# Performance work log

Hardware: AMD Instinct MI355X
Metric: run time of the kernel (lower is better)

The kernel has to match this reference:

```python
import jax, jax.numpy as jnp
import numpy as np

B, S, D, H = 8, 1024, 768, 12
DH = D // H


def setup_inputs() -> dict:
    key = jax.random.key(0)
    ks = jax.random.split(key, 6)
    scale = 1.0 / np.sqrt(D)
    return {
        "inputs": jax.random.normal(ks[0], (B, S, D), dtype=jnp.float32),
        "Wq": jax.random.normal(ks[1], (D, D), dtype=jnp.float32) * scale,
        "bq": jnp.zeros((D,), jnp.float32),
        "Wk": jax.random.normal(ks[2], (D, D), dtype=jnp.float32) * scale,
        "bk": jnp.zeros((D,), jnp.float32),
        "Wv": jax.random.normal(ks[3], (D, D), dtype=jnp.float32) * scale,
        "bv": jnp.zeros((D,), jnp.float32),
        "Wo": jax.random.normal(ks[4], (D, D), dtype=jnp.float32) * scale,
        "bo": jnp.zeros((D,), jnp.float32),
    }


def _split_heads(x):
    # [B,S,D] -> [B,H,S,DH]
    b, s, _ = x.shape
    return x.reshape(b, s, H, DH).transpose(0, 2, 1, 3)


def reference(inputs, Wq, bq, Wk, bk, Wv, bv, Wo, bo):
    q = _split_heads(inputs @ Wq + bq)
    k = _split_heads(inputs @ Wk + bk)
    v = _split_heads(inputs @ Wv + bv)
    # scaled dot-product attention; scale = sqrt(projection_dim)
    scores = jnp.einsum("bhqd,bhkd->bhqk", q, k) / jnp.sqrt(jnp.float32(DH))
    weights = jax.nn.softmax(scores, axis=-1)
    attn = jnp.einsum("bhqk,bhkd->bhqd", weights, v)
    attn = attn.transpose(0, 2, 1, 3).reshape(inputs.shape[0], -1, D)
    return attn @ Wo + bo
```

## Files before the change

### kernel.cpp

```cpp
#include <hip/hip_runtime.h>
#include <math.h>

#define B 8
#define S 1024
#define D 768
#define H 12
#define DH 64
#define M_TOT (B * S)

#define QSCALE 0.18033688011112042f

typedef short bf16x8 __attribute__((ext_vector_type(8)));
typedef float f32x4 __attribute__((ext_vector_type(4)));
typedef unsigned u32x4 __attribute__((ext_vector_type(4)));

__device__ __forceinline__ unsigned short f2bf(float x) {
    unsigned u = __builtin_bit_cast(unsigned, x);
    u = (u + 0x7FFFu + ((u >> 16) & 1u)) >> 16;
    return (unsigned short)u;
}
__device__ __forceinline__ unsigned short f2bf_ru(float x) {
    return (unsigned short)((__builtin_bit_cast(unsigned, x) + 0x8000u) >> 16);
}
__device__ __forceinline__ unsigned pk2bf_ru(float a, float b) {
    unsigned ua = __builtin_bit_cast(unsigned, a) + 0x8000u;
    unsigned ub = __builtin_bit_cast(unsigned, b) + 0x8000u;
    return __builtin_amdgcn_perm(ub, ua, 0x07060302u);
}

__device__ __forceinline__ void async16(const unsigned short* g, unsigned short* l) {
    __builtin_amdgcn_global_load_lds((const __attribute__((address_space(1))) void*)g,
                                     (__attribute__((address_space(3))) void*)l, 16, 0, 0);
}

__device__ __forceinline__ void stage_tiles(const unsigned short* __restrict__ A,
                                            const unsigned short* __restrict__ Bt,
                                            unsigned short* At, unsigned short* Bs,
                                            int m0, int n0, int k0, int w, int srow, int scol) {
#pragma unroll
    for (int c = 0; c < 2; ++c) {
        const int cc = w * 2 + c;
        const int row = cc * 16 + srow;
        async16(&A[(size_t)(m0 + row) * D + k0 + scol], &At[cc * 512]);
        async16(&Bt[(size_t)(n0 + row) * D + k0 + scol], &Bs[cc * 512]);
    }
}

__global__ __launch_bounds__(256) void prep(const float* __restrict__ inputs,
                                            unsigned short* __restrict__ Abf,
                                            const float* W0, const float* W1,
                                            const float* W2, const float* W3,
                                            unsigned short* T0, unsigned short* T1,
                                            unsigned short* T2, unsigned short* T3) {
    const int bid = blockIdx.x;
    const int t = threadIdx.x;
    if (bid < 6144) {
        const int i = (bid * 256 + t) * 4;
        const float4 v = *(const float4*)&inputs[i];
        ushort4 o;
        o.x = f2bf(v.x); o.y = f2bf(v.y); o.z = f2bf(v.z); o.w = f2bf(v.w);
        *(ushort4*)&Abf[i] = o;
    } else {
        const int id = bid - 6144;
        const int z = id / 144;
        const int rem = id % 144;
        const int kx = rem % 12, ny = rem / 12;
        const float* Wsrc[4] = {W0, W1, W2, W3};
        unsigned short* Tdst[4] = {T0, T1, T2, T3};
        const float* Wm = Wsrc[z];
        unsigned short* Tm = Tdst[z];
        __shared__ float tile[64][65];
        const int r = t >> 4, c4 = (t & 15) * 4;
        const int k0 = kx * 64, n0 = ny * 64;
#pragma unroll
        for (int rr = 0; rr < 4; ++rr) {
            const float4 v = *(const float4*)&Wm[(size_t)(k0 + r + rr * 16) * D + n0 + c4];
            tile[r + rr * 16][c4 + 0] = v.x;
            tile[r + rr * 16][c4 + 1] = v.y;
            tile[r + rr * 16][c4 + 2] = v.z;
            tile[r + rr * 16][c4 + 3] = v.w;
        }
        __syncthreads();
#pragma unroll
        for (int rr = 0; rr < 4; ++rr) {
            const int nr = r + rr * 16;
            ushort4 o;
            o.x = f2bf(tile[c4 + 0][nr]);
            o.y = f2bf(tile[c4 + 1][nr]);
            o.z = f2bf(tile[c4 + 2][nr]);
            o.w = f2bf(tile[c4 + 3][nr]);
            *(ushort4*)&Tm[(size_t)(n0 + nr) * D + k0 + c4] = o;
        }
    }
}

__global__ __launch_bounds__(256) void gemm_qkv(const unsigned short* __restrict__ A,
                                                const unsigned short* __restrict__ Wtq,
                                                const unsigned short* __restrict__ Wtk,
                                                const unsigned short* __restrict__ Wtv,
                                                const float* __restrict__ bq,
                                                const float* __restrict__ bk,
                                                const float* __restrict__ bv,
                                                unsigned short* __restrict__ Qb,
                                                unsigned short* __restrict__ Kb,
                                                unsigned short* __restrict__ Vtb) {
    __shared__ unsigned short At[2][128 * 32];
    __shared__ unsigned short Bs[2][128 * 32];
    const int z = blockIdx.z;
    const unsigned short* Bt = (z == 0) ? Wtq : (z == 1) ? Wtk : Wtv;
    const float* bias = (z == 0) ? bq : (z == 1) ? bk : bv;
    const float scale = (z == 0) ? QSCALE : 1.0f;

    const int t = threadIdx.x;
    const int w = t >> 6, lane = t & 63;
    const int quad = lane >> 4, l15 = lane & 15;
    const int m0 = blockIdx.x * 128, n0 = blockIdx.y * 128;
    const int wm = (w & 1) * 64, wn = (w >> 1) * 64;
    const int srow = lane >> 2, scol = (lane & 3) * 8;

    f32x4 acc[4][4];
#pragma unroll
    for (int i = 0; i < 4; ++i)
#pragma unroll
        for (int j = 0; j < 4; ++j) acc[i][j] = (f32x4){0.f, 0.f, 0.f, 0.f};

    stage_tiles(A, Bt, At[0], Bs[0], m0, n0, 0, w, srow, scol);
    for (int kt = 0; kt < D / 32; ++kt) {
        unsigned short* Atc = At[kt & 1];
        unsigned short* Bsc = Bs[kt & 1];
        if (kt + 1 < D / 32) {
            stage_tiles(A, Bt, At[(kt + 1) & 1], Bs[(kt + 1) & 1], m0, n0, (kt + 1) * 32, w, srow, scol);
            __asm__ volatile("s_waitcnt vmcnt(4)" ::: "memory");
        } else {
            __asm__ volatile("s_waitcnt vmcnt(0)" ::: "memory");
        }
        __asm__ volatile("s_barrier" ::: "memory");
        bf16x8 af[4], bfr[4];
#pragma unroll
        for (int i = 0; i < 4; ++i)
            af[i] = *(const bf16x8*)&Atc[(wm + i * 16 + l15) * 32 + quad * 8];
#pragma unroll
        for (int j = 0; j < 4; ++j)
            bfr[j] = *(const bf16x8*)&Bsc[(wn + j * 16 + l15) * 32 + quad * 8];
#pragma unroll
        for (int i = 0; i < 4; ++i)
#pragma unroll
            for (int j = 0; j < 4; ++j)
                acc[i][j] = __builtin_amdgcn_mfma_f32_16x16x32_bf16(af[i], bfr[j], acc[i][j], 0, 0, 0);
        __asm__ volatile("s_barrier" ::: "memory");
    }

#pragma unroll
    for (int j = 0; j < 4; ++j) {
        const int col = n0 + wn + j * 16 + l15;
        const float bv2 = bias[col];
#pragma unroll
        for (int i = 0; i < 4; ++i) {
            const int row0 = m0 + wm + i * 16 + quad * 4;
            if (z < 2) {
                unsigned short* C = (z == 0) ? Qb : Kb;
#pragma unroll
                for (int r = 0; r < 4; ++r)
                    C[(size_t)(row0 + r) * D + col] = f2bf_ru((acc[i][j][r] + bv2) * scale);
            } else {
                const int h = col >> 6, dh = col & 63;
                const int bb = row0 >> 10, s0 = row0 & 1023;
                const int g = (s0 & 63) >> 2;
                const int kap = ((g >> 3) << 5) | ((g & 3) << 3) | (((g >> 2) & 1) << 2);
                const int s0p = (s0 & ~63) | kap;
                uint2 u;
                u.x = pk2bf_ru(acc[i][j][0] + bv2, acc[i][j][1] + bv2);
                u.y = pk2bf_ru(acc[i][j][2] + bv2, acc[i][j][3] + bv2);
                *(uint2*)&Vtb[((size_t)(bb * H + h) * DH + dh) * S + s0p] = u;
            }
        }
    }
}

__global__ __launch_bounds__(256) void gemm_out(const unsigned short* __restrict__ A,
                                                const unsigned short* __restrict__ Bt,
                                                const float* __restrict__ bias,
                                                float* __restrict__ C) {
    __shared__ unsigned short At[2][128 * 32];
    __shared__ unsigned short Bs[2][128 * 32];
    const int t = threadIdx.x;
    const int w = t >> 6, lane = t & 63;
    const int quad = lane >> 4, l15 = lane & 15;
    const int m0 = blockIdx.x * 128, n0 = blockIdx.y * 128;
    const int wm = (w & 1) * 64, wn = (w >> 1) * 64;
    const int srow = lane >> 2, scol = (lane & 3) * 8;

    f32x4 acc[4][4];
#pragma unroll
    for (int i = 0; i < 4; ++i)
#pragma unroll
        for (int j = 0; j < 4; ++j) acc[i][j] = (f32x4){0.f, 0.f, 0.f, 0.f};

    stage_tiles(A, Bt, At[0], Bs[0], m0, n0, 0, w, srow, scol);
    for (int kt = 0; kt < D / 32; ++kt) {
        unsigned short* Atc = At[kt & 1];
        unsigned short* Bsc = Bs[kt & 1];
        if (kt + 1 < D / 32) {
            stage_tiles(A, Bt, At[(kt + 1) & 1], Bs[(kt + 1) & 1], m0, n0, (kt + 1) * 32, w, srow, scol);
            __asm__ volatile("s_waitcnt vmcnt(4)" ::: "memory");
        } else {
            __asm__ volatile("s_waitcnt vmcnt(0)" ::: "memory");
        }
        __asm__ volatile("s_barrier" ::: "memory");
        bf16x8 af[4], bfr[4];
#pragma unroll
        for (int i = 0; i < 4; ++i)
            af[i] = *(const bf16x8*)&Atc[(wm + i * 16 + l15) * 32 + quad * 8];
#pragma unroll
        for (int j = 0; j < 4; ++j)
            bfr[j] = *(const bf16x8*)&Bsc[(wn + j * 16 + l15) * 32 + quad * 8];
#pragma unroll
        for (int i = 0; i < 4; ++i)
#pragma unroll
            for (int j = 0; j < 4; ++j)
                acc[i][j] = __builtin_amdgcn_mfma_f32_16x16x32_bf16(af[i], bfr[j], acc[i][j], 0, 0, 0);
        __asm__ volatile("s_barrier" ::: "memory");
    }

#pragma unroll
    for (int j = 0; j < 4; ++j) {
        const int col = n0 + wn + j * 16 + l15;
        const float bv = bias[col];
#pragma unroll
        for (int i = 0; i < 4; ++i) {
            const int row0 = m0 + wm + i * 16 + quad * 4;
#pragma unroll
            for (int r = 0; r < 4; ++r) C[(size_t)(row0 + r) * D + col] = acc[i][j][r] + bv;
        }
    }
}

__global__ __launch_bounds__(256) void attn_mfma(const unsigned short* __restrict__ Qg,
                                                 const unsigned short* __restrict__ Kg,
                                                 const unsigned short* __restrict__ Vtg,
                                                 unsigned short* __restrict__ ATT) {
    __shared__ unsigned short Ks[2][2 * 64 * 32];
    __shared__ unsigned short Vs[2][2 * 64 * 32];

    const int t = threadIdx.x;
    const int w = t >> 6, lane = t & 63;
    const int quad = lane >> 4, l15 = lane & 15;
    const int bh = blockIdx.x % (B * H);
    const int q0 = (blockIdx.x / (B * H)) * 128;
    const int b = bh / H, h = bh % H;

    bf16x8 qb[2][2];
#pragma unroll
    for (int qh = 0; qh < 2; ++qh) {
        const size_t qoff = ((size_t)(b * S + q0 + w * 32 + qh * 16 + l15)) * D + h * DH;
        qb[qh][0] = *(const bf16x8*)&Qg[qoff + quad * 8];
        qb[qh][1] = *(const bf16x8*)&Qg[qoff + 32 + quad * 8];
    }

    f32x4 o[2][4];
#pragma unroll
    for (int qh = 0; qh < 2; ++qh)
#pragma unroll
        for (int n = 0; n < 4; ++n) o[qh][n] = (f32x4){0.f, 0.f, 0.f, 0.f};
    float l_acc[2] = {0.f, 0.f};

    const int srow = lane >> 2;
    const int scol = (((lane & 3) ^ ((lane >> 3) & 3))) * 8;
    const int fsw = ((quad ^ ((l15 >> 1) & 3)) * 8);

    #define STAGE(ktv, bf)                                                                   \
        {                                                                                     \
            const int _kt = (ktv);                                                            \
            _Pragma("unroll")                                                                 \
            for (int kc = 0; kc < 2; ++kc) {                                                  \
                async16(&Kg[((size_t)(b * S + _kt * 64 + w * 16 + srow)) * D + h * DH + kc * 32 + scol], \
                        &Ks[bf][kc * 2048 + w * 512]);                                        \
                async16(&Vtg[((size_t)(bh * DH + w * 16 + srow)) * S + _kt * 64 + kc * 32 + scol],       \
                        &Vs[bf][kc * 2048 + w * 512]);                                        \
            }                                                                                 \
        }

    STAGE(0, 0);
    for (int kt = 0; kt < S / 64; ++kt) {
        const int buf = kt & 1;
        if (kt + 1 < S / 64) {
            STAGE(kt + 1, buf ^ 1);
            __asm__ volatile("s_waitcnt vmcnt(4)" ::: "memory");
        } else {
            __asm__ volatile("s_waitcnt vmcnt(0)" ::: "memory");
        }
        __asm__ volatile("s_barrier" ::: "memory");

        f32x4 sc[2][4];
#pragma unroll
        for (int n = 0; n < 4; ++n) {
            const bf16x8 ka0 = *(const bf16x8*)&Ks[buf][0 * 2048 + (n * 16 + l15) * 32 + fsw];
            const bf16x8 ka1 = *(const bf16x8*)&Ks[buf][1 * 2048 + (n * 16 + l15) * 32 + fsw];
#pragma unroll
            for (int qh = 0; qh < 2; ++qh) {
                f32x4 zz = (f32x4){0.f, 0.f, 0.f, 0.f};
                zz = __builtin_amdgcn_mfma_f32_16x16x32_bf16(ka0, qb[qh][0], zz, 0, 0, 0);
                zz = __builtin_amdgcn_mfma_f32_16x16x32_bf16(ka1, qb[qh][1], zz, 0, 0, 0);
                sc[qh][n] = zz;
            }
        }

        bf16x8 pb[2][2];
#pragma unroll
        for (int qh = 0; qh < 2; ++qh) {
            float p[4][4];
            float rs = 0.f;
#pragma unroll
            for (int n = 0; n < 4; ++n) {
#pragma unroll
                for (int r = 0; r < 4; ++r) {
                    p[n][r] = __builtin_amdgcn_exp2f(sc[qh][n][r]);
                    rs += p[n][r];
                }
            }
            l_acc[qh] += rs;
            u32x4 u0, u1;
            u0.x = pk2bf_ru(p[0][0], p[0][1]);
            u0.y = pk2bf_ru(p[0][2], p[0][3]);
            u0.z = pk2bf_ru(p[1][0], p[1][1]);
            u0.w = pk2bf_ru(p[1][2], p[1][3]);
            u1.x = pk2bf_ru(p[2][0], p[2][1]);
            u1.y = pk2bf_ru(p[2][2], p[2][3]);
            u1.z = pk2bf_ru(p[3][0], p[3][1]);
            u1.w = pk2bf_ru(p[3][2], p[3][3]);
            pb[qh][0] = __builtin_bit_cast(bf16x8, u0);
            pb[qh][1] = __builtin_bit_cast(bf16x8, u1);
        }

#pragma unroll
        for (int n = 0; n < 4; ++n) {
            const bf16x8 va0 = *(const bf16x8*)&Vs[buf][0 * 2048 + (n * 16 + l15) * 32 + fsw];
            const bf16x8 va1 = *(const bf16x8*)&Vs[buf][1 * 2048 + (n * 16 + l15) * 32 + fsw];
#pragma unroll
            for (int qh = 0; qh < 2; ++qh) {
                o[qh][n] = __builtin_amdgcn_mfma_f32_16x16x32_bf16(va0, pb[qh][0], o[qh][n], 0, 0, 0);
                o[qh][n] = __builtin_amdgcn_mfma_f32_16x16x32_bf16(va1, pb[qh][1], o[qh][n], 0, 0, 0);
            }
        }
        __asm__ volatile("s_barrier" ::: "memory");
    }
    #undef STAGE

#pragma unroll
    for (int qh = 0; qh < 2; ++qh) {
        float l = l_acc[qh];
        l += __shfl_xor(l, 16, 64);
        l += __shfl_xor(l, 32, 64);
        const float inv = 1.0f / l;
        const size_t row = (size_t)(b * S + q0 + w * 32 + qh * 16 + l15) * D + h * DH;
#pragma unroll
        for (int n = 0; n < 4; ++n) {
            uint2 u;
            u.x = pk2bf_ru(o[qh][n][0] * inv, o[qh][n][1] * inv);
            u.y = pk2bf_ru(o[qh][n][2] * inv, o[qh][n][3] * inv);
            *(uint2*)&ATT[row + n * 16 + quad * 4] = u;
        }
    }
}

extern "C" void kernel_launch(void* const* d_in, const int* in_sizes, int n_in,
                              void* d_out, int out_size, void* d_ws, size_t ws_size,
                              hipStream_t stream) {
    const float* inputs = (const float*)d_in[0];
    const float* Wq = (const float*)d_in[1];
    const float* bq = (const float*)d_in[2];
    const float* Wk = (const float*)d_in[3];
    const float* bk = (const float*)d_in[4];
    const float* Wv = (const float*)d_in[5];
    const float* bv = (const float*)d_in[6];
    const float* Wo = (const float*)d_in[7];
    const float* bo = (const float*)d_in[8];

    const size_t nA = (size_t)M_TOT * D;
    unsigned short* Abf  = (unsigned short*)d_ws;
    unsigned short* Qb   = Abf + nA;
    unsigned short* Kb   = Qb + nA;
    unsigned short* Vtb  = Kb + nA;
    unsigned short* ATTb = Vtb + nA;
    unsigned short* Wtq  = ATTb + nA;
    unsigned short* Wtk  = Wtq + (size_t)D * D;
    unsigned short* Wtv  = Wtk + (size_t)D * D;
    unsigned short* Wto  = Wtv + (size_t)D * D;

    prep<<<6144 + 576, 256, 0, stream>>>(inputs, Abf, Wq, Wk, Wv, Wo, Wtq, Wtk, Wtv, Wto);

    gemm_qkv<<<dim3(M_TOT / 128, D / 128, 3), 256, 0, stream>>>(
        Abf, Wtq, Wtk, Wtv, bq, bk, bv, Qb, Kb, Vtb);

    attn_mfma<<<dim3((S / 128) * B * H), 256, 0, stream>>>(Qb, Kb, Vtb, ATTb);

    gemm_out<<<dim3(M_TOT / 128, D / 128), 256, 0, stream>>>(ATTb, Wto, bo, (float*)d_out);
}
```

Before: 202.7 us.

## Triple-buffer LDS tiles and drop trailing barrier in GEMM and attention loops

Switches the QKV GEMM, output GEMM and attention kernels from double to triple buffering of shared-memory tiles. Two tiles are prefetched before the loop, and the prefetch for step kt+2 is issued after the barrier, which makes the end-of-iteration barrier unnecessary. The aim is to hide more global-load latency and remove one barrier per iteration. In exchange, LDS use per block grows by half, which may reduce occupancy.

```diff
diff --git a/kernel.cpp b/kernel.cpp
--- a/kernel.cpp
+++ b/kernel.cpp
@@ -104,8 +104,8 @@
                                                 unsigned short* __restrict__ Qb,
                                                 unsigned short* __restrict__ Kb,
                                                 unsigned short* __restrict__ Vtb) {
-    __shared__ unsigned short At[2][128 * 32];
-    __shared__ unsigned short Bs[2][128 * 32];
+    __shared__ unsigned short At[3][128 * 32];
+    __shared__ unsigned short Bs[3][128 * 32];
     const int z = blockIdx.z;
     const unsigned short* Bt = (z == 0) ? Wtq : (z == 1) ? Wtk : Wtv;
     const float* bias = (z == 0) ? bq : (z == 1) ? bk : bv;
@@ -117,6 +117,7 @@
     const int m0 = blockIdx.x * 128, n0 = blockIdx.y * 128;
     const int wm = (w & 1) * 64, wn = (w >> 1) * 64;
     const int srow = lane >> 2, scol = (lane & 3) * 8;
+    const int NT = D / 32;
 
     f32x4 acc[4][4];
 #pragma unroll
@@ -125,16 +126,22 @@
         for (int j = 0; j < 4; ++j) acc[i][j] = (f32x4){0.f, 0.f, 0.f, 0.f};
 
     stage_tiles(A, Bt, At[0], Bs[0], m0, n0, 0, w, srow, scol);
-    for (int kt = 0; kt < D / 32; ++kt) {
-        unsigned short* Atc = At[kt & 1];
-        unsigned short* Bsc = Bs[kt & 1];
-        if (kt + 1 < D / 32) {
-            stage_tiles(A, Bt, At[(kt + 1) & 1], Bs[(kt + 1) & 1], m0, n0, (kt + 1) * 32, w, srow, scol);
+    stage_tiles(A, Bt, At[1], Bs[1], m0, n0, 32, w, srow, scol);
+    int cur = 0, nxt = 2;
+    for (int kt = 0; kt < NT; ++kt) {
+        if (kt + 1 < NT) {
             __asm__ volatile("s_waitcnt vmcnt(4)" ::: "memory");
         } else {
             __asm__ volatile("s_waitcnt vmcnt(0)" ::: "memory");
         }
         __asm__ volatile("s_barrier" ::: "memory");
+        if (kt + 2 < NT) {
+            stage_tiles(A, Bt, At[nxt], Bs[nxt], m0, n0, (kt + 2) * 32, w, srow, scol);
+            nxt = (nxt == 2) ? 0 : nxt + 1;
+        }
+        const unsigned short* Atc = At[cur];
+        const unsigned short* Bsc = Bs[cur];
+        cur = (cur == 2) ? 0 : cur + 1;
         bf16x8 af[4], bfr[4];
 #pragma unroll
         for (int i = 0; i < 4; ++i)
@@ -147,7 +154,6 @@
 #pragma unroll
             for (int j = 0; j < 4; ++j)
                 acc[i][j] = __builtin_amdgcn_mfma_f32_16x16x32_bf16(af[i], bfr[j], acc[i][j], 0, 0, 0);
-        __asm__ volatile("s_barrier" ::: "memory");
     }
 
 #pragma unroll
@@ -181,14 +187,15 @@
                                                 const unsigned short* __restrict__ Bt,
                                                 const float* __restrict__ bias,
                                                 float* __restrict__ C) {
-    __shared__ unsigned short At[2][128 * 32];
-    __shared__ unsigned short Bs[2][128 * 32];
+    __shared__ unsigned short At[3][128 * 32];
+    __shared__ unsigned short Bs[3][128 * 32];
     const int t = threadIdx.x;
     const int w = t >> 6, lane = t & 63;
     const int quad = lane >> 4, l15 = lane & 15;
     const int m0 = blockIdx.x * 128, n0 = blockIdx.y * 128;
     const int wm = (w & 1) * 64, wn = (w >> 1) * 64;
     const int srow = lane >> 2, scol = (lane & 3) * 8;
+    const int NT = D / 32;
 
     f32x4 acc[4][4];
 #pragma unroll
@@ -197,16 +204,22 @@
         for (int j = 0; j < 4; ++j) acc[i][j] = (f32x4){0.f, 0.f, 0.f, 0.f};
 
     stage_tiles(A, Bt, At[0], Bs[0], m0, n0, 0, w, srow, scol);
-    for (int kt = 0; kt < D / 32; ++kt) {
-        unsigned short* Atc = At[kt & 1];
-        unsigned short* Bsc = Bs[kt & 1];
-        if (kt + 1 < D / 32) {
-            stage_tiles(A, Bt, At[(kt + 1) & 1], Bs[(kt + 1) & 1], m0, n0, (kt + 1) * 32, w, srow, scol);
+    stage_tiles(A, Bt, At[1], Bs[1], m0, n0, 32, w, srow, scol);
+    int cur = 0, nxt = 2;
+    for (int kt = 0; kt < NT; ++kt) {
+        if (kt + 1 < NT) {
             __asm__ volatile("s_waitcnt vmcnt(4)" ::: "memory");
         } else {
             __asm__ volatile("s_waitcnt vmcnt(0)" ::: "memory");
         }
         __asm__ volatile("s_barrier" ::: "memory");
+        if (kt + 2 < NT) {
+            stage_tiles(A, Bt, At[nxt], Bs[nxt], m0, n0, (kt + 2) * 32, w, srow, scol);
+            nxt = (nxt == 2) ? 0 : nxt + 1;
+        }
+        const unsigned short* Atc = At[cur];
+        const unsigned short* Bsc = Bs[cur];
+        cur = (cur == 2) ? 0 : cur + 1;
         bf16x8 af[4], bfr[4];
 #pragma unroll
         for (int i = 0; i < 4; ++i)
@@ -219,7 +232,6 @@
 #pragma unroll
             for (int j = 0; j < 4; ++j)
                 acc[i][j] = __builtin_amdgcn_mfma_f32_16x16x32_bf16(af[i], bfr[j], acc[i][j], 0, 0, 0);
-        __asm__ volatile("s_barrier" ::: "memory");
     }
 
 #pragma unroll
@@ -239,8 +251,8 @@
                                                  const unsigned short* __restrict__ Kg,
                                                  const unsigned short* __restrict__ Vtg,
                                                  unsigned short* __restrict__ ATT) {
-    __shared__ unsigned short Ks[2][2 * 64 * 32];
-    __shared__ unsigned short Vs[2][2 * 64 * 32];
+    __shared__ unsigned short Ks[3][2 * 64 * 32];
+    __shared__ unsigned short Vs[3][2 * 64 * 32];
 
     const int t = threadIdx.x;
     const int w = t >> 6, lane = t & 63;
@@ -267,6 +279,7 @@
     const int srow = lane >> 2;
     const int scol = (((lane & 3) ^ ((lane >> 3) & 3))) * 8;
     const int fsw = ((quad ^ ((l15 >> 1) & 3)) * 8);
+    const int NT = S / 64;
 
     #define STAGE(ktv, bf)                                                                   \
         {                                                                                     \
@@ -281,15 +294,21 @@
         }
 
     STAGE(0, 0);
-    for (int kt = 0; kt < S / 64; ++kt) {
-        const int buf = kt & 1;
-        if (kt + 1 < S / 64) {
-            STAGE(kt + 1, buf ^ 1);
+    STAGE(1, 1);
+    int cur = 0, nxt = 2;
+    for (int kt = 0; kt < NT; ++kt) {
+        if (kt + 1 < NT) {
             __asm__ volatile("s_waitcnt vmcnt(4)" ::: "memory");
         } else {
             __asm__ volatile("s_waitcnt vmcnt(0)" ::: "memory");
         }
         __asm__ volatile("s_barrier" ::: "memory");
+        if (kt + 2 < NT) {
+            STAGE(kt + 2, nxt);
+            nxt = (nxt == 2) ? 0 : nxt + 1;
+        }
+        const int buf = cur;
+        cur = (cur == 2) ? 0 : cur + 1;
 
         f32x4 sc[2][4];
 #pragma unroll
@@ -342,7 +361,6 @@
                 o[qh][n] = __builtin_amdgcn_mfma_f32_16x16x32_bf16(va1, pb[qh][1], o[qh][n], 0, 0, 0);
             }
         }
-        __asm__ volatile("s_barrier" ::: "memory");
     }
     #undef STAGE
 
```

After: 199.1 us. About the same (-1.8%).
